# Kernel tuning notes

Measured on AMD Instinct MI355X. Metric: run time of the kernel, lower is better.

The kernel has to match this reference:

```python
import jax, jax.numpy as jnp
import numpy as np

N = 131072
DIMS_IN = 16
DIMS_C = 16
UNITS = 512
BINS = 10
MIN_W = 1e-3   # min_bin_width
MIN_H = 1e-3   # min_bin_height
MIN_D = 1e-3   # min_bin_derivative
N_PERMS = 4                 # ceil(log2(DIMS_IN))
BLOCKS = 2 * N_PERMS        # log permutation strategy doubles each bit-mask
DT = DIMS_IN // 2           # transformed dims per block (power-of-2 => exact half)
FEAT_IN = DT + DIMS_C       # subnet input features
FEAT_OUT = DT * (3 * BINS + 1)  # widths+heights+derivatives per transformed dim


def _masks():
    # Reproduces the 'log' permutation mask construction from Flow.__init__
    cm = np.array([[int(b) for b in np.binary_repr(j, N_PERMS)] for j in range(DIMS_IN)])
    cm = cm[:, ::-1].astype(bool).T           # (N_PERMS, DIMS_IN)
    m = np.repeat(cm, 2, axis=0)              # (BLOCKS, DIMS_IN)
    m[1::2] = ~m[1::2]
    return m  # True = condition dim, False = transformed dim


def _mlp(h, W0, b0, W1, b1, W2, b2):
    # layers=3 -> Linear/ReLU/Linear/ReLU/Linear
    h = jax.nn.relu(h @ W0 + b0)
    h = jax.nn.relu(h @ W1 + b1)
    return h @ W2 + b2


def _rqs_forward(x, uw, uh, ud):
    # x: (n, DT) in [0,1]; uw/uh: (n, DT, BINS); ud: (n, DT, BINS+1)
    w = MIN_W + (1.0 - MIN_W * BINS) * jax.nn.softmax(uw, axis=-1)
    h = MIN_H + (1.0 - MIN_H * BINS) * jax.nn.softmax(uh, axis=-1)
    d = MIN_D + jax.nn.softplus(ud)
    zero = jnp.zeros(w.shape[:-1] + (1,), w.dtype)
    cw = jnp.concatenate([zero, jnp.cumsum(w, axis=-1)], axis=-1)  # knot x-positions
    ch = jnp.concatenate([zero, jnp.cumsum(h, axis=-1)], axis=-1)  # knot y-positions
    # bin search: index of bin containing x
    idx = jnp.clip(jnp.sum(x[..., None] >= cw, axis=-1) - 1, 0, BINS - 1)
    take = lambda a, i: jnp.take_along_axis(a, i[..., None], axis=-1)[..., 0]
    xk, wk = take(cw, idx), take(w, idx)
    yk, hk = take(ch, idx), take(h, idx)
    dk, dk1 = take(d, idx), take(d, idx + 1)
    theta = jnp.clip((x - xk) / wk, 0.0, 1.0)
    s = hk / wk
    t1 = theta * (1.0 - theta)
    denom = s + (dk1 + dk - 2.0 * s) * t1
    y = yk + hk * (s * theta * theta + dk * t1) / denom
    logdet = (2.0 * jnp.log(s)
              + jnp.log(dk1 * theta * theta + 2.0 * s * t1 + dk * (1.0 - theta) ** 2)
              - 2.0 * jnp.log(denom))
    return y, logdet


def _log_prob(x, c, W0, b0, W1, b1, W2, b2):
    masks = _masks()
    z = x
    logdet = jnp.zeros(x.shape[0], x.dtype)
    for b in range(BLOCKS):
        m = masks[b]
        cond_idx = np.where(m)[0]
        trans_idx = np.where(~m)[0]
        subnet_in = jnp.concatenate([z[:, cond_idx], c], axis=-1)  # (n, FEAT_IN)
        params = _mlp(subnet_in, W0[b], b0[b], W1[b], b1[b], W2[b], b2[b])
        params = params.reshape(-1, DT, 3 * BINS + 1)
        uw, uh, ud = params[..., :BINS], params[..., BINS:2 * BINS], params[..., 2 * BINS:]
        y, lj = _rqs_forward(z[:, trans_idx], uw, uh, ud)
        logdet = logdet + jnp.sum(lj, axis=-1)
        z = z.at[:, trans_idx].set(y)
    # uniform latent on [0,1]^d => latent log-density is 0
    return logdet


def setup_inputs() -> dict:
    key = jax.random.key(0)
    ks = jax.random.split(key, 6)
    x = jax.random.uniform(ks[0], (N, DIMS_IN), jnp.float32)
    c = jax.random.normal(ks[1], (N, DIMS_C), jnp.float32)
    W0 = jax.random.normal(ks[2], (BLOCKS, FEAT_IN, UNITS), jnp.float32) / np.sqrt(FEAT_IN)
    W1 = jax.random.normal(ks[3], (BLOCKS, UNITS, UNITS), jnp.float32) / np.sqrt(UNITS)
    W2 = jax.random.normal(ks[4], (BLOCKS, UNITS, FEAT_OUT), jnp.float32) / np.sqrt(UNITS)
    b0 = jnp.zeros((BLOCKS, UNITS), jnp.float32)
    b1 = jnp.zeros((BLOCKS, UNITS), jnp.float32)
    b2 = jnp.zeros((BLOCKS, FEAT_OUT), jnp.float32)
    return {"x": x, "c": c, "W0": W0, "b0": b0, "W1": W1, "b1": b1, "W2": W2, "b2": b2}


def reference(x, c, W0, b0, W1, b1, W2, b2):
    return _log_prob(x, c, W0, b0, W1, b1, W2, b2)
```

## Files before the change

### kernel.cpp

```cpp
#include <hip/hip_runtime.h>
#include <math.h>

#define NROWS 131072
#define DIN   16
#define DC    16
#define UNITS 512
#define BINS  10
#define DT    8
#define FOUT  248
#define M_TILE 64
#define NWG   (NROWS / M_TILE)

#define Z_OFF    0u
#define W0F_OFF  8388608u
#define W1F_OFF  8650752u
#define W2F_OFF  12845056u

typedef _Float16 h16x8 __attribute__((ext_vector_type(8)));
typedef float    f32x4 __attribute__((ext_vector_type(4)));

union Frag { h16x8 v; uint4 q; unsigned int u32[4]; _Float16 h[8]; };

static __device__ inline unsigned int pack2h(float lo, float hi) {
    union { _Float16 h[2]; unsigned int u; } x;
    x.h[0] = (_Float16)lo; x.h[1] = (_Float16)hi;
    return x.u;
}

static __device__ inline float fast_rcp(float x) { return __builtin_amdgcn_rcpf(x); }

__global__ __launch_bounds__(256)
void prep_weights(const float* __restrict__ W0, const float* __restrict__ W1,
                  const float* __restrict__ W2, _Float16* __restrict__ W0F,
                  _Float16* __restrict__ W1F, _Float16* __restrict__ W2F)
{
    const int idx = blockIdx.x * 256 + threadIdx.x;
    const int SZ0 = 8 * 32 * 512;
    const int SZ1 = 8 * 32 * 16 * 512;
    const int SZ2 = 8 * 16 * 4 * 4 * 512;
    if (idx < SZ0) {
        int b = idx >> 14, r = idx & 16383;
        int ut = r >> 9, le = r & 511;
        int lane = le >> 3, j = le & 7;
        int quad = lane >> 4, l15 = lane & 15;
        int m = ut * 16 + l15, k = quad * 8 + j;
        W0F[idx] = (k < 24) ? (_Float16)W0[b * (24 * 512) + k * 512 + m] : (_Float16)0.f;
    } else if (idx < SZ0 + SZ1) {
        int i = idx - SZ0;
        int b = i >> 18, r = i & 262143;
        int ut = r >> 13, r2 = r & 8191;
        int ks = r2 >> 9, le = r2 & 511;
        int lane = le >> 3, j = le & 7;
        int quad = lane >> 4, l15 = lane & 15;
        int m = ut * 16 + l15, k = ks * 32 + quad * 8 + j;
        W1F[i] = (_Float16)W1[(b << 18) + k * 512 + m];
    } else if (idx < SZ0 + SZ1 + SZ2) {
        int i = idx - SZ0 - SZ1;
        int b = i >> 17, r = i & 131071;
        int ut2 = r >> 13, r2 = r & 8191;
        int c2 = r2 >> 11, r3 = r2 & 2047;
        int ks2 = r3 >> 9, le = r3 & 511;
        int lane = le >> 3, j = le & 7;
        int quad = lane >> 4, l15 = lane & 15;
        int m = ut2 * 16 + l15, k = c2 * 128 + ks2 * 32 + quad * 8 + j;
        W2F[i] = (m < FOUT) ? (_Float16)W2[b * (512 * FOUT) + k * FOUT + m] : (_Float16)0.f;
    }
}

__global__ __launch_bounds__(512, 4)
void flow_block_kernel(const float* __restrict__ z, const float* __restrict__ c,
                       const _Float16* __restrict__ W0F, const float* __restrict__ b0,
                       const _Float16* __restrict__ W1F, const float* __restrict__ b1,
                       const _Float16* __restrict__ W2F, const float* __restrict__ b2,
                       float* __restrict__ zout, float* __restrict__ logdet,
                       int p, int inv)
{
    __shared__ __align__(16) char smem[65536];

    const int t    = threadIdx.x;
    const int wave = t >> 6;
    const int lane = t & 63;
    const int quad = lane >> 4;
    const int l15  = lane & 15;
    const int row0 = blockIdx.x * M_TILE;
    const int lowmask = (1 << p) - 1;
    const int cv = 1 - inv, tv = inv;
    const int lofs = lane * 8;

    Frag bx[4];
    #pragma unroll
    for (int rt = 0; rt < 4; ++rt) {
        const int n = rt * 16 + l15;
        const float* zr = z + (size_t)(row0 + n) * DIN;
        const float* cr = c + (size_t)(row0 + n) * DC;
        float v[8];
        if (quad == 0) {
            #pragma unroll
            for (int j = 0; j < 8; ++j) {
                const int col = ((j >> p) << (p + 1)) | (cv << p) | (j & lowmask);
                v[j] = zr[col];
            }
        } else if (quad == 1) {
            #pragma unroll
            for (int j = 0; j < 8; ++j) v[j] = cr[j];
        } else if (quad == 2) {
            #pragma unroll
            for (int j = 0; j < 8; ++j) v[j] = cr[8 + j];
        } else {
            #pragma unroll
            for (int j = 0; j < 8; ++j) v[j] = 0.f;
        }
        #pragma unroll
        for (int j = 0; j < 4; ++j) bx[rt].u32[j] = pack2h(v[2 * j], v[2 * j + 1]);
    }

    #pragma unroll
    for (int j = 0; j < 4; ++j) {
        const int ut = wave * 4 + j;
        Frag a; a.q = *(const uint4*)(W0F + (ut << 9) + lofs);
        const f32x4 bias = *(const f32x4*)(b0 + ut * 16 + quad * 4);
        const int m0 = ut * 16 + quad * 4;
        #pragma unroll
        for (int rt = 0; rt < 4; ++rt) {
            f32x4 acc = __builtin_amdgcn_mfma_f32_16x16x32_f16(a.v, bx[rt].v, bias, 0, 0, 0);
            const int n = rt * 16 + l15;
            uint2 w2;
            w2.x = pack2h(fmaxf(acc.x, 0.f), fmaxf(acc.y, 0.f));
            w2.y = pack2h(fmaxf(acc.z, 0.f), fmaxf(acc.w, 0.f));
            const int addr = n * 1024 + (((m0 >> 3) ^ (n & 7)) * 16) + ((m0 & 4) * 2);
            *(uint2*)(smem + addr) = w2;
        }
    }
    __syncthreads();

    f32x4 h1[4][4];
    #pragma unroll
    for (int j = 0; j < 4; ++j) {
        const int ut = wave * 4 + j;
        const f32x4 bias = *(const f32x4*)(b1 + ut * 16 + quad * 4);
        #pragma unroll
        for (int rt = 0; rt < 4; ++rt) h1[j][rt] = bias;
    }
    #pragma unroll 2
    for (int ks = 0; ks < 16; ++ks) {
        Frag B[4];
        #pragma unroll
        for (int rt = 0; rt < 4; ++rt) {
            const int n = rt * 16 + l15;
            B[rt].v = *(const h16x8*)(smem + n * 1024 + (((ks * 4 + quad) ^ (n & 7)) * 16));
        }
        #pragma unroll
        for (int j = 0; j < 4; ++j) {
            const int ut = wave * 4 + j;
            Frag a; a.q = *(const uint4*)(W1F + (((ut << 4) + ks) << 9) + lofs);
            #pragma unroll
            for (int rt = 0; rt < 4; ++rt)
                h1[j][rt] = __builtin_amdgcn_mfma_f32_16x16x32_f16(a.v, B[rt].v, h1[j][rt], 0, 0, 0);
        }
    }
    __syncthreads();

    #pragma unroll
    for (int j = 0; j < 4; ++j) {
        const int ut = wave * 4 + j;
        const int m0 = ut * 16 + quad * 4;
        #pragma unroll
        for (int rt = 0; rt < 4; ++rt) {
            const int n = rt * 16 + l15;
            uint2 w2;
            w2.x = pack2h(fmaxf(h1[j][rt].x, 0.f), fmaxf(h1[j][rt].y, 0.f));
            w2.y = pack2h(fmaxf(h1[j][rt].z, 0.f), fmaxf(h1[j][rt].w, 0.f));
            const int addr = n * 1024 + (((m0 >> 3) ^ (n & 7)) * 16) + ((m0 & 4) * 2);
            *(uint2*)(smem + addr) = w2;
        }
    }
    __syncthreads();

    f32x4 pacc[2][4];
    #pragma unroll
    for (int i2 = 0; i2 < 2; ++i2) {
        const int m0 = (wave * 2 + i2) * 16 + quad * 4;
        f32x4 bias;
        if (m0 < FOUT) bias = *(const f32x4*)(b2 + m0);
        else { bias.x = 0.f; bias.y = 0.f; bias.z = 0.f; bias.w = 0.f; }
        #pragma unroll
        for (int rt = 0; rt < 4; ++rt) pacc[i2][rt] = bias;
    }
    #pragma unroll 2
    for (int kk = 0; kk < 16; ++kk) {
        const int kc = kk * 4 + quad;
        Frag B[4];
        #pragma unroll
        for (int rt = 0; rt < 4; ++rt) {
            const int n = rt * 16 + l15;
            B[rt].v = *(const h16x8*)(smem + n * 1024 + ((kc ^ (n & 7)) * 16));
        }
        #pragma unroll
        for (int i2 = 0; i2 < 2; ++i2) {
            const int ut2 = wave * 2 + i2;
            Frag a; a.q = *(const uint4*)(W2F + (((ut2 << 4) + kk) << 9) + lofs);
            #pragma unroll
            for (int rt = 0; rt < 4; ++rt)
                pacc[i2][rt] = __builtin_amdgcn_mfma_f32_16x16x32_f16(a.v, B[rt].v, pacc[i2][rt], 0, 0, 0);
        }
    }
    __syncthreads();

    #pragma unroll
    for (int i2 = 0; i2 < 2; ++i2) {
        const int m0 = (wave * 2 + i2) * 16 + quad * 4;
        if (m0 < FOUT) {
            #pragma unroll
            for (int rt = 0; rt < 4; ++rt) {
                const int n = rt * 16 + l15;
                *(f32x4*)(smem + n * 1008 + m0 * 4) = pacc[i2][rt];
            }
        }
    }
    __syncthreads();

    {
        const int r = t >> 3;
        const int d = t & 7;
        const int row = row0 + r;
        const int td = ((d >> p) << (p + 1)) | (tv << p) | (d & lowmask);

        const float x = z[(size_t)row * DIN + td];

        const float* pp = (const float*)(smem + r * 1008) + d * 31;
        float pv[31];
        #pragma unroll
        for (int i = 0; i < 31; ++i) pv[i] = pp[i];

        float mw = pv[0];
        #pragma unroll
        for (int i = 1; i < BINS; ++i) mw = fmaxf(mw, pv[i]);
        float w[BINS]; float sw = 0.f;
        #pragma unroll
        for (int i = 0; i < BINS; ++i) { w[i] = __expf(pv[i] - mw); sw += w[i]; }
        const float rw = (1.0f - 0.001f * BINS) * fast_rcp(sw);
        #pragma unroll
        for (int i = 0; i < BINS; ++i) w[i] = 0.001f + rw * w[i];

        float mh = pv[BINS];
        #pragma unroll
        for (int i = 1; i < BINS; ++i) mh = fmaxf(mh, pv[BINS + i]);
        float hh[BINS]; float sh = 0.f;
        #pragma unroll
        for (int i = 0; i < BINS; ++i) { hh[i] = __expf(pv[BINS + i] - mh); sh += hh[i]; }
        const float rh = (1.0f - 0.001f * BINS) * fast_rcp(sh);
        #pragma unroll
        for (int i = 0; i < BINS; ++i) hh[i] = 0.001f + rh * hh[i];

        float dd[BINS + 1];
        #pragma unroll
        for (int i = 0; i < BINS + 1; ++i) {
            const float u = pv[2 * BINS + i];
            dd[i] = 0.001f + fmaxf(u, 0.f) + __logf(1.f + __expf(-fabsf(u)));
        }

        float cw[BINS], ch[BINS];
        cw[0] = 0.f; ch[0] = 0.f;
        #pragma unroll
        for (int i = 0; i < BINS - 1; ++i) { cw[i + 1] = cw[i] + w[i]; ch[i + 1] = ch[i] + hh[i]; }

        float xk = cw[0], wk = w[0], yk = ch[0], hk = hh[0], dk = dd[0], dk1 = dd[1];
        #pragma unroll
        for (int i = 1; i < BINS; ++i) {
            const bool sel = (x >= cw[i]);
            xk  = sel ? cw[i]     : xk;
            wk  = sel ? w[i]      : wk;
            yk  = sel ? ch[i]     : yk;
            hk  = sel ? hh[i]     : hk;
            dk  = sel ? dd[i]     : dk;
            dk1 = sel ? dd[i + 1] : dk1;
        }

        const float inv_wk = fast_rcp(wk);
        float th = (x - xk) * inv_wk;
        th = fminf(fmaxf(th, 0.f), 1.f);
        const float s   = hk * inv_wk;
        const float t1  = th * (1.f - th);
        const float den = s + (dk1 + dk - 2.f * s) * t1;
        const float inv_den = fast_rcp(den);
        const float num = s * th * th + dk * t1;
        const float y   = yk + hk * num * inv_den;
        const float om  = 1.f - th;
        const float r1  = s * inv_den;
        const float q   = r1 * r1 * (dk1 * th * th + 2.f * s * t1 + dk * om * om);
        float ljv = __logf(q);

        zout[(size_t)row * DIN + td] = y;

        float v = ljv;
        v += __shfl_down(v, 4, 8);
        v += __shfl_down(v, 2, 8);
        v += __shfl_down(v, 1, 8);
        if ((t & 7) == 0) logdet[row0 + (t >> 3)] += v;
    }
}

extern "C" void kernel_launch(void* const* d_in, const int* in_sizes, int n_in,
                              void* d_out, int out_size, void* d_ws, size_t ws_size,
                              hipStream_t stream) {
    (void)in_sizes; (void)n_in; (void)out_size; (void)ws_size;
    const float* x  = (const float*)d_in[0];
    const float* c  = (const float*)d_in[1];
    const float* W0 = (const float*)d_in[2];
    const float* b0 = (const float*)d_in[3];
    const float* W1 = (const float*)d_in[4];
    const float* b1 = (const float*)d_in[5];
    const float* W2 = (const float*)d_in[6];
    const float* b2 = (const float*)d_in[7];
    float* out = (float*)d_out;

    char* ws = (char*)d_ws;
    float* z = (float*)(ws + Z_OFF);
    _Float16* W0F = (_Float16*)(ws + W0F_OFF);
    _Float16* W1F = (_Float16*)(ws + W1F_OFF);
    _Float16* W2F = (_Float16*)(ws + W2F_OFF);

    hipMemcpyAsync(z, x, (size_t)NROWS * DIN * sizeof(float),
                   hipMemcpyDeviceToDevice, stream);
    hipMemsetAsync(out, 0, (size_t)NROWS * sizeof(float), stream);

    prep_weights<<<12800, 256, 0, stream>>>(W0, W1, W2, W0F, W1F, W2F);

    dim3 grid(NWG), block(512);
    for (int b = 0; b < 8; ++b) {
        const int p = b >> 1, inv = b & 1;
        flow_block_kernel<<<grid, block, 0, stream>>>(
            z, c,
            W0F + (size_t)b * 32 * 512,          b0 + (size_t)b * UNITS,
            W1F + (size_t)b * 32 * 16 * 512,     b1 + (size_t)b * UNITS,
            W2F + (size_t)b * 16 * 4 * 4 * 512,  b2 + (size_t)b * FOUT,
            z, out, p, inv);
    }
}
```

Baseline: 1.087 ms.

## Fuse all eight flow blocks into one kernel with z held in LDS

Replaces the eight per-block kernel launches with a single kernel that loops over all coupling blocks. Each workgroup keeps its 64x16 z tile in shared memory, packs the conditioning inputs once, and accumulates logdet in registers, writing it once at the end. This removes the device-to-device copy, the memset, seven launches and the global z round trips between blocks. The cost is an extra LDS array on top of 64KB, which may reduce occupancy, plus a longer-running kernel per workgroup.

Result: slower. 1.208 ms (+11.1%).

```diff
diff --git a/kernel.cpp b/kernel.cpp
--- a/kernel.cpp
+++ b/kernel.cpp
@@ -11,10 +11,9 @@
 #define M_TILE 64
 #define NWG   (NROWS / M_TILE)
 
-#define Z_OFF    0u
-#define W0F_OFF  8388608u
-#define W1F_OFF  8650752u
-#define W2F_OFF  12845056u
+#define W0F_OFF  0u
+#define W1F_OFF  262144u
+#define W2F_OFF  4456448u
 
 typedef _Float16 h16x8 __attribute__((ext_vector_type(8)));
 typedef float    f32x4 __attribute__((ext_vector_type(4)));
@@ -68,14 +67,14 @@
 }
 
 __global__ __launch_bounds__(512, 4)
-void flow_block_kernel(const float* __restrict__ z, const float* __restrict__ c,
-                       const _Float16* __restrict__ W0F, const float* __restrict__ b0,
-                       const _Float16* __restrict__ W1F, const float* __restrict__ b1,
-                       const _Float16* __restrict__ W2F, const float* __restrict__ b2,
-                       float* __restrict__ zout, float* __restrict__ logdet,
-                       int p, int inv)
+void flow_fused(const float* __restrict__ x, const float* __restrict__ c,
+                const _Float16* __restrict__ W0F, const float* __restrict__ b0,
+                const _Float16* __restrict__ W1F, const float* __restrict__ b1,
+                const _Float16* __restrict__ W2F, const float* __restrict__ b2,
+                float* __restrict__ logdet)
 {
     __shared__ __align__(16) char smem[65536];
+    __shared__ float zt[64][17];
 
     const int t    = threadIdx.x;
     const int wave = t >> 6;
@@ -83,24 +82,22 @@
     const int quad = lane >> 4;
     const int l15  = lane & 15;
     const int row0 = blockIdx.x * M_TILE;
-    const int lowmask = (1 << p) - 1;
-    const int cv = 1 - inv, tv = inv;
     const int lofs = lane * 8;
 
-    Frag bx[4];
+    {
+        const float* xr = x + (size_t)row0 * DIN;
+        const int i0 = t, i1 = t + 512;
+        zt[i0 >> 4][i0 & 15] = xr[i0];
+        zt[i1 >> 4][i1 & 15] = xr[i1];
+    }
+
+    unsigned int cpk[4][4];
     #pragma unroll
     for (int rt = 0; rt < 4; ++rt) {
         const int n = rt * 16 + l15;
-        const float* zr = z + (size_t)(row0 + n) * DIN;
         const float* cr = c + (size_t)(row0 + n) * DC;
         float v[8];
-        if (quad == 0) {
-            #pragma unroll
-            for (int j = 0; j < 8; ++j) {
-                const int col = ((j >> p) << (p + 1)) | (cv << p) | (j & lowmask);
-                v[j] = zr[col];
-            }
-        } else if (quad == 1) {
+        if (quad == 1) {
             #pragma unroll
             for (int j = 0; j < 8; ++j) v[j] = cr[j];
         } else if (quad == 2) {
@@ -111,193 +108,229 @@
             for (int j = 0; j < 8; ++j) v[j] = 0.f;
         }
         #pragma unroll
-        for (int j = 0; j < 4; ++j) bx[rt].u32[j] = pack2h(v[2 * j], v[2 * j + 1]);
+        for (int j = 0; j < 4; ++j) cpk[rt][j] = pack2h(v[2 * j], v[2 * j + 1]);
     }
 
-    #pragma unroll
-    for (int j = 0; j < 4; ++j) {
-        const int ut = wave * 4 + j;
-        Frag a; a.q = *(const uint4*)(W0F + (ut << 9) + lofs);
-        const f32x4 bias = *(const f32x4*)(b0 + ut * 16 + quad * 4);
-        const int m0 = ut * 16 + quad * 4;
+    float ldacc = 0.f;
+    __syncthreads();
+
+    for (int b = 0; b < 8; ++b) {
+        const int p = b >> 1, inv = b & 1;
+        const int lowmask = (1 << p) - 1;
+        const int cv = 1 - inv, tv = inv;
+        const _Float16* W0Fb = W0F + (size_t)b * (32 * 512);
+        const _Float16* W1Fb = W1F + (size_t)b * (32 * 16 * 512);
+        const _Float16* W2Fb = W2F + (size_t)b * (16 * 4 * 4 * 512);
+        const float* b0b = b0 + b * UNITS;
+        const float* b1b = b1 + b * UNITS;
+        const float* b2b = b2 + b * FOUT;
+
+        Frag bx[4];
         #pragma unroll
         for (int rt = 0; rt < 4; ++rt) {
-            f32x4 acc = __builtin_amdgcn_mfma_f32_16x16x32_f16(a.v, bx[rt].v, bias, 0, 0, 0);
-            const int n = rt * 16 + l15;
-            uint2 w2;
-            w2.x = pack2h(fmaxf(acc.x, 0.f), fmaxf(acc.y, 0.f));
-            w2.y = pack2h(fmaxf(acc.z, 0.f), fmaxf(acc.w, 0.f));
-            const int addr = n * 1024 + (((m0 >> 3) ^ (n & 7)) * 16) + ((m0 & 4) * 2);
-            *(uint2*)(smem + addr) = w2;
-        }
-    }
-    __syncthreads();
-
-    f32x4 h1[4][4];
-    #pragma unroll
-    for (int j = 0; j < 4; ++j) {
-        const int ut = wave * 4 + j;
-        const f32x4 bias = *(const f32x4*)(b1 + ut * 16 + quad * 4);
-        #pragma unroll
-        for (int rt = 0; rt < 4; ++rt) h1[j][rt] = bias;
-    }
-    #pragma unroll 2
-    for (int ks = 0; ks < 16; ++ks) {
-        Frag B[4];
-        #pragma unroll
-        for (int rt = 0; rt < 4; ++rt) {
-            const int n = rt * 16 + l15;
-            B[rt].v = *(const h16x8*)(smem + n * 1024 + (((ks * 4 + quad) ^ (n & 7)) * 16));
-        }
+            if (quad == 0) {
+                const int n = rt * 16 + l15;
+                float v[8];
+                #pragma unroll
+                for (int j = 0; j < 8; ++j) {
+                    const int col = ((j >> p) << (p + 1)) | (cv << p) | (j & lowmask);
+                    v[j] = zt[n][col];
+                }
+                #pragma unroll
+                for (int j = 0; j < 4; ++j) bx[rt].u32[j] = pack2h(v[2 * j], v[2 * j + 1]);
+            } else {
+                #pragma unroll
+                for (int j = 0; j < 4; ++j) bx[rt].u32[j] = cpk[rt][j];
+            }
+        }
+
         #pragma unroll
         for (int j = 0; j < 4; ++j) {
             const int ut = wave * 4 + j;
-            Frag a; a.q = *(const uint4*)(W1F + (((ut << 4) + ks) << 9) + lofs);
-            #pragma unroll
-            for (int rt = 0; rt < 4; ++rt)
-                h1[j][rt] = __builtin_amdgcn_mfma_f32_16x16x32_f16(a.v, B[rt].v, h1[j][rt], 0, 0, 0);
-        }
+            Frag a; a.q = *(const uint4*)(W0Fb + (ut << 9) + lofs);
+            const f32x4 bias = *(const f32x4*)(b0b + ut * 16 + quad * 4);
+            const int m0 = ut * 16 + quad * 4;
+            #pragma unroll
+            for (int rt = 0; rt < 4; ++rt) {
+                f32x4 acc = __builtin_amdgcn_mfma_f32_16x16x32_f16(a.v, bx[rt].v, bias, 0, 0, 0);
+                const int n = rt * 16 + l15;
+                uint2 w2;
+                w2.x = pack2h(fmaxf(acc.x, 0.f), fmaxf(acc.y, 0.f));
+                w2.y = pack2h(fmaxf(acc.z, 0.f), fmaxf(acc.w, 0.f));
+                const int addr = n * 1024 + (((m0 >> 3) ^ (n & 7)) * 16) + ((m0 & 4) * 2);
+                *(uint2*)(smem + addr) = w2;
+            }
+        }
+        __syncthreads();
+
+        f32x4 h1[4][4];
+        #pragma unroll
+        for (int j = 0; j < 4; ++j) {
+            const int ut = wave * 4 + j;
+            const f32x4 bias = *(const f32x4*)(b1b + ut * 16 + quad * 4);
+            #pragma unroll
+            for (int rt = 0; rt < 4; ++rt) h1[j][rt] = bias;
+        }
+        #pragma unroll 2
+        for (int ks = 0; ks < 16; ++ks) {
+            Frag B[4];
+            #pragma unroll
+            for (int rt = 0; rt < 4; ++rt) {
+                const int n = rt * 16 + l15;
+                B[rt].v = *(const h16x8*)(smem + n * 1024 + (((ks * 4 + quad) ^ (n & 7)) * 16));
+            }
+            #pragma unroll
+            for (int j = 0; j < 4; ++j) {
+                const int ut = wave * 4 + j;
+                Frag a; a.q = *(const uint4*)(W1Fb + (((ut << 4) + ks) << 9) + lofs);
+                #pragma unroll
+                for (int rt = 0; rt < 4; ++rt)
+                    h1[j][rt] = __builtin_amdgcn_mfma_f32_16x16x32_f16(a.v, B[rt].v, h1[j][rt], 0, 0, 0);
+            }
+        }
+        __syncthreads();
+
+        #pragma unroll
+        for (int j = 0; j < 4; ++j) {
+            const int ut = wave * 4 + j;
+            const int m0 = ut * 16 + quad * 4;
+            #pragma unroll
+            for (int rt = 0; rt < 4; ++rt) {
+                const int n = rt * 16 + l15;
+                uint2 w2;
+                w2.x = pack2h(fmaxf(h1[j][rt].x, 0.f), fmaxf(h1[j][rt].y, 0.f));
+                w2.y = pack2h(fmaxf(h1[j][rt].z, 0.f), fmaxf(h1[j][rt].w, 0.f));
+                const int addr = n * 1024 + (((m0 >> 3) ^ (n & 7)) * 16) + ((m0 & 4) * 2);
+                *(uint2*)(smem + addr) = w2;
+            }
+        }
+        __syncthreads();
+
+        f32x4 pacc[2][4];
+        #pragma unroll
+        for (int i2 = 0; i2 < 2; ++i2) {
+            const int m0 = (wave * 2 + i2) * 16 + quad * 4;
+            f32x4 bias;
+            if (m0 < FOUT) bias = *(const f32x4*)(b2b + m0);
+            else { bias.x = 0.f; bias.y = 0.f; bias.z = 0.f; bias.w = 0.f; }
+            #pragma unroll
+            for (int rt = 0; rt < 4; ++rt) pacc[i2][rt] = bias;
+        }
+        #pragma unroll 2
+        for (int kk = 0; kk < 16; ++kk) {
+            const int kc = kk * 4 + quad;
+            Frag B[4];
+            #pragma unroll
+            for (int rt = 0; rt < 4; ++rt) {
+                const int n = rt * 16 + l15;
+                B[rt].v = *(const h16x8*)(smem + n * 1024 + ((kc ^ (n & 7)) * 16));
+            }
+            #pragma unroll
+            for (int i2 = 0; i2 < 2; ++i2) {
+                const int ut2 = wave * 2 + i2;
+                Frag a; a.q = *(const uint4*)(W2Fb + (((ut2 << 4) + kk) << 9) + lofs);
+                #pragma unroll
+                for (int rt = 0; rt < 4; ++rt)
+                    pacc[i2][rt] = __builtin_amdgcn_mfma_f32_16x16x32_f16(a.v, B[rt].v, pacc[i2][rt], 0, 0, 0);
+            }
+        }
+        __syncthreads();
+
+        #pragma unroll
+        for (int i2 = 0; i2 < 2; ++i2) {
+            const int m0 = (wave * 2 + i2) * 16 + quad * 4;
+            if (m0 < FOUT) {
+                #pragma unroll
+                for (int rt = 0; rt < 4; ++rt) {
+                    const int n = rt * 16 + l15;
+                    *(f32x4*)(smem + n * 1008 + m0 * 4) = pacc[i2][rt];
+                }
+            }
+        }
+        __syncthreads();
+
+        {
+            const int r = t >> 3;
+            const int d = t & 7;
+            const int td = ((d >> p) << (p + 1)) | (tv << p) | (d & lowmask);
+
+            const float xv = zt[r][td];
+
+            const float* pp = (const float*)(smem + r * 1008) + d * 31;
+            float pv[31];
+            #pragma unroll
+            for (int i = 0; i < 31; ++i) pv[i] = pp[i];
+
+            float mw = pv[0];
+            #pragma unroll
+            for (int i = 1; i < BINS; ++i) mw = fmaxf(mw, pv[i]);
+            float w[BINS]; float sw = 0.f;
+            #pragma unroll
+            for (int i = 0; i < BINS; ++i) { w[i] = __expf(pv[i] - mw); sw += w[i]; }
+            const float rw = (1.0f - 0.001f * BINS) * fast_rcp(sw);
+            #pragma unroll
+            for (int i = 0; i < BINS; ++i) w[i] = 0.001f + rw * w[i];
+
+            float mh = pv[BINS];
+            #pragma unroll
+            for (int i = 1; i < BINS; ++i) mh = fmaxf(mh, pv[BINS + i]);
+            float hh[BINS]; float sh = 0.f;
+            #pragma unroll
+            for (int i = 0; i < BINS; ++i) { hh[i] = __expf(pv[BINS + i] - mh); sh += hh[i]; }
+            const float rh = (1.0f - 0.001f * BINS) * fast_rcp(sh);
+            #pragma unroll
+            for (int i = 0; i < BINS; ++i) hh[i] = 0.001f + rh * hh[i];
+
+            float dd[BINS + 1];
+            #pragma unroll
+            for (int i = 0; i < BINS + 1; ++i) {
+                const float u = pv[2 * BINS + i];
+                dd[i] = 0.001f + fmaxf(u, 0.f) + __logf(1.f + __expf(-fabsf(u)));
+            }
+
+            float cw[BINS], ch[BINS];
+            cw[0] = 0.f; ch[0] = 0.f;
+            #pragma unroll
+            for (int i = 0; i < BINS - 1; ++i) { cw[i + 1] = cw[i] + w[i]; ch[i + 1] = ch[i] + hh[i]; }
+
+            float xk = cw[0], wk = w[0], yk = ch[0], hk = hh[0], dk = dd[0], dk1 = dd[1];
+            #pragma unroll
+            for (int i = 1; i < BINS; ++i) {
+                const bool sel = (xv >= cw[i]);
+                xk  = sel ? cw[i]     : xk;
+                wk  = sel ? w[i]      : wk;
+                yk  = sel ? ch[i]     : yk;
+                hk  = sel ? hh[i]     : hk;
+                dk  = sel ? dd[i]     : dk;
+                dk1 = sel ? dd[i + 1] : dk1;
+            }
+
+            const float inv_wk = fast_rcp(wk);
+            float th = (xv - xk) * inv_wk;
+            th = fminf(fmaxf(th, 0.f), 1.f);
+            const float s   = hk * inv_wk;
+            const float t1  = th * (1.f - th);
+            const float den = s + (dk1 + dk - 2.f * s) * t1;
+            const float inv_den = fast_rcp(den);
+            const float num = s * th * th + dk * t1;
+            const float y   = yk + hk * num * inv_den;
+            const float om  = 1.f - th;
+            const float r1  = s * inv_den;
+            const float q   = r1 * r1 * (dk1 * th * th + 2.f * s * t1 + dk * om * om);
+            float ljv = __logf(q);
+
+            zt[r][td] = y;
+
+            float v = ljv;
+            v += __shfl_down(v, 4, 8);
+            v += __shfl_down(v, 2, 8);
+            v += __shfl_down(v, 1, 8);
+            if ((t & 7) == 0) ldacc += v;
+        }
+        __syncthreads();
     }
-    __syncthreads();
-
-    #pragma unroll
-    for (int j = 0; j < 4; ++j) {
-        const int ut = wave * 4 + j;
-        const int m0 = ut * 16 + quad * 4;
-        #pragma unroll
-        for (int rt = 0; rt < 4; ++rt) {
-            const int n = rt * 16 + l15;
-            uint2 w2;
-            w2.x = pack2h(fmaxf(h1[j][rt].x, 0.f), fmaxf(h1[j][rt].y, 0.f));
-            w2.y = pack2h(fmaxf(h1[j][rt].z, 0.f), fmaxf(h1[j][rt].w, 0.f));
-            const int addr = n * 1024 + (((m0 >> 3) ^ (n & 7)) * 16) + ((m0 & 4) * 2);
-            *(uint2*)(smem + addr) = w2;
-        }
-    }
-    __syncthreads();
-
-    f32x4 pacc[2][4];
-    #pragma unroll
-    for (int i2 = 0; i2 < 2; ++i2) {
-        const int m0 = (wave * 2 + i2) * 16 + quad * 4;
-        f32x4 bias;
-        if (m0 < FOUT) bias = *(const f32x4*)(b2 + m0);
-        else { bias.x = 0.f; bias.y = 0.f; bias.z = 0.f; bias.w = 0.f; }
-        #pragma unroll
-        for (int rt = 0; rt < 4; ++rt) pacc[i2][rt] = bias;
-    }
-    #pragma unroll 2
-    for (int kk = 0; kk < 16; ++kk) {
-        const int kc = kk * 4 + quad;
-        Frag B[4];
-        #pragma unroll
-        for (int rt = 0; rt < 4; ++rt) {
-            const int n = rt * 16 + l15;
-            B[rt].v = *(const h16x8*)(smem + n * 1024 + ((kc ^ (n & 7)) * 16));
-        }
-        #pragma unroll
-        for (int i2 = 0; i2 < 2; ++i2) {
-            const int ut2 = wave * 2 + i2;
-            Frag a; a.q = *(const uint4*)(W2F + (((ut2 << 4) + kk) << 9) + lofs);
-            #pragma unroll
-            for (int rt = 0; rt < 4; ++rt)
-                pacc[i2][rt] = __builtin_amdgcn_mfma_f32_16x16x32_f16(a.v, B[rt].v, pacc[i2][rt], 0, 0, 0);
-        }
-    }
-    __syncthreads();
-
-    #pragma unroll
-    for (int i2 = 0; i2 < 2; ++i2) {
-        const int m0 = (wave * 2 + i2) * 16 + quad * 4;
-        if (m0 < FOUT) {
-            #pragma unroll
-            for (int rt = 0; rt < 4; ++rt) {
-                const int n = rt * 16 + l15;
-                *(f32x4*)(smem + n * 1008 + m0 * 4) = pacc[i2][rt];
-            }
-        }
-    }
-    __syncthreads();
-
-    {
-        const int r = t >> 3;
-        const int d = t & 7;
-        const int row = row0 + r;
-        const int td = ((d >> p) << (p + 1)) | (tv << p) | (d & lowmask);
-
-        const float x = z[(size_t)row * DIN + td];
-
-        const float* pp = (const float*)(smem + r * 1008) + d * 31;
-        float pv[31];
-        #pragma unroll
-        for (int i = 0; i < 31; ++i) pv[i] = pp[i];
-
-        float mw = pv[0];
-        #pragma unroll
-        for (int i = 1; i < BINS; ++i) mw = fmaxf(mw, pv[i]);
-        float w[BINS]; float sw = 0.f;
-        #pragma unroll
-        for (int i = 0; i < BINS; ++i) { w[i] = __expf(pv[i] - mw); sw += w[i]; }
-        const float rw = (1.0f - 0.001f * BINS) * fast_rcp(sw);
-        #pragma unroll
-        for (int i = 0; i < BINS; ++i) w[i] = 0.001f + rw * w[i];
-
-        float mh = pv[BINS];
-        #pragma unroll
-        for (int i = 1; i < BINS; ++i) mh = fmaxf(mh, pv[BINS + i]);
-        float hh[BINS]; float sh = 0.f;
-        #pragma unroll
-        for (int i = 0; i < BINS; ++i) { hh[i] = __expf(pv[BINS + i] - mh); sh += hh[i]; }
-        const float rh = (1.0f - 0.001f * BINS) * fast_rcp(sh);
-        #pragma unroll
-        for (int i = 0; i < BINS; ++i) hh[i] = 0.001f + rh * hh[i];
-
-        float dd[BINS + 1];
-        #pragma unroll
-        for (int i = 0; i < BINS + 1; ++i) {
-            const float u = pv[2 * BINS + i];
-            dd[i] = 0.001f + fmaxf(u, 0.f) + __logf(1.f + __expf(-fabsf(u)));
-        }
-
-        float cw[BINS], ch[BINS];
-        cw[0] = 0.f; ch[0] = 0.f;
-        #pragma unroll
-        for (int i = 0; i < BINS - 1; ++i) { cw[i + 1] = cw[i] + w[i]; ch[i + 1] = ch[i] + hh[i]; }
-
-        float xk = cw[0], wk = w[0], yk = ch[0], hk = hh[0], dk = dd[0], dk1 = dd[1];
-        #pragma unroll
-        for (int i = 1; i < BINS; ++i) {
-            const bool sel = (x >= cw[i]);
-            xk  = sel ? cw[i]     : xk;
-            wk  = sel ? w[i]      : wk;
-            yk  = sel ? ch[i]     : yk;
-            hk  = sel ? hh[i]     : hk;
-            dk  = sel ? dd[i]     : dk;
-            dk1 = sel ? dd[i + 1] : dk1;
-        }
-
-        const float inv_wk = fast_rcp(wk);
-        float th = (x - xk) * inv_wk;
-        th = fminf(fmaxf(th, 0.f), 1.f);
-        const float s   = hk * inv_wk;
-        const float t1  = th * (1.f - th);
-        const float den = s + (dk1 + dk - 2.f * s) * t1;
-        const float inv_den = fast_rcp(den);
-        const float num = s * th * th + dk * t1;
-        const float y   = yk + hk * num * inv_den;
-        const float om  = 1.f - th;
-        const float r1  = s * inv_den;
-        const float q   = r1 * r1 * (dk1 * th * th + 2.f * s * t1 + dk * om * om);
-        float ljv = __logf(q);
-
-        zout[(size_t)row * DIN + td] = y;
-
-        float v = ljv;
-        v += __shfl_down(v, 4, 8);
-        v += __shfl_down(v, 2, 8);
-        v += __shfl_down(v, 1, 8);
-        if ((t & 7) == 0) logdet[row0 + (t >> 3)] += v;
-    }
+
+    if ((t & 7) == 0) logdet[row0 + (t >> 3)] = ldacc;
 }
 
 extern "C" void kernel_launch(void* const* d_in, const int* in_sizes, int n_in,
@@ -315,25 +348,12 @@
     float* out = (float*)d_out;
 
     char* ws = (char*)d_ws;
-    float* z = (float*)(ws + Z_OFF);
     _Float16* W0F = (_Float16*)(ws + W0F_OFF);
     _Float16* W1F = (_Float16*)(ws + W1F_OFF);
     _Float16* W2F = (_Float16*)(ws + W2F_OFF);
 
-    hipMemcpyAsync(z, x, (size_t)NROWS * DIN * sizeof(float),
-                   hipMemcpyDeviceToDevice, stream);
-    hipMemsetAsync(out, 0, (size_t)NROWS * sizeof(float), stream);
-
     prep_weights<<<12800, 256, 0, stream>>>(W0, W1, W2, W0F, W1F, W2F);
 
-    dim3 grid(NWG), block(512);
-    for (int b = 0; b < 8; ++b) {
-        const int p = b >> 1, inv = b & 1;
-        flow_block_kernel<<<grid, block, 0, stream>>>(
-            z, c,
-            W0F + (size_t)b * 32 * 512,          b0 + (size_t)b * UNITS,
-            W1F + (size_t)b * 32 * 16 * 512,     b1 + (size_t)b * UNITS,
-            W2F + (size_t)b * 16 * 4 * 4 * 512,  b2 + (size_t)b * FOUT,
-            z, out, p, inv);
-    }
+    flow_fused<<<dim3(NWG), dim3(512), 0, stream>>>(
+        x, c, W0F, b0, W1F, b1, W2F, b2, out);
 }
```

## Fuse all eight flow blocks into one persistent kernel with MFMA priority hints

Applied to the files above, without the earlier changes.

Replaces the eight per-block kernel launches with a single persistent kernel of 512 workgroups. Each workgroup owns a fixed set of row tiles and loops over all eight coupling blocks. Because each row's data dependency stays inside one workgroup, no grid-wide sync is needed, and launch gaps and tail effects between blocks go away. It also wraps the MFMA inner loops in s_setprio. The trade-off is less parallelism: 512 workgroups of 512 threads, each processing four tiles serially per block, may underfill the GPU compared with 2048 workgroups per launch.

Measured after the change: 1.469 ms. 1.35x slower.

```diff
diff --git a/kernel.cpp b/kernel.cpp
--- a/kernel.cpp
+++ b/kernel.cpp
@@ -9,7 +9,9 @@
 #define DT    8
 #define FOUT  248
 #define M_TILE 64
-#define NWG   (NROWS / M_TILE)
+#define NTILES (NROWS / M_TILE)
+#define PWG   512
+#define TPW   (NTILES / PWG)
 
 #define Z_OFF    0u
 #define W0F_OFF  8388608u
@@ -68,12 +70,11 @@
 }
 
 __global__ __launch_bounds__(512, 4)
-void flow_block_kernel(const float* __restrict__ z, const float* __restrict__ c,
-                       const _Float16* __restrict__ W0F, const float* __restrict__ b0,
-                       const _Float16* __restrict__ W1F, const float* __restrict__ b1,
-                       const _Float16* __restrict__ W2F, const float* __restrict__ b2,
-                       float* __restrict__ zout, float* __restrict__ logdet,
-                       int p, int inv)
+void flow_persist(const float* __restrict__ zin, const float* __restrict__ c,
+                  const _Float16* __restrict__ W0F, const float* __restrict__ b0,
+                  const _Float16* __restrict__ W1F, const float* __restrict__ b1,
+                  const _Float16* __restrict__ W2F, const float* __restrict__ b2,
+                  float* __restrict__ zout, float* __restrict__ logdet)
 {
     __shared__ __align__(16) char smem[65536];
 
@@ -82,221 +83,239 @@
     const int lane = t & 63;
     const int quad = lane >> 4;
     const int l15  = lane & 15;
-    const int row0 = blockIdx.x * M_TILE;
-    const int lowmask = (1 << p) - 1;
-    const int cv = 1 - inv, tv = inv;
     const int lofs = lane * 8;
 
-    Frag bx[4];
-    #pragma unroll
-    for (int rt = 0; rt < 4; ++rt) {
-        const int n = rt * 16 + l15;
-        const float* zr = z + (size_t)(row0 + n) * DIN;
-        const float* cr = c + (size_t)(row0 + n) * DC;
-        float v[8];
-        if (quad == 0) {
-            #pragma unroll
-            for (int j = 0; j < 8; ++j) {
-                const int col = ((j >> p) << (p + 1)) | (cv << p) | (j & lowmask);
-                v[j] = zr[col];
-            }
-        } else if (quad == 1) {
-            #pragma unroll
-            for (int j = 0; j < 8; ++j) v[j] = cr[j];
-        } else if (quad == 2) {
-            #pragma unroll
-            for (int j = 0; j < 8; ++j) v[j] = cr[8 + j];
-        } else {
-            #pragma unroll
-            for (int j = 0; j < 8; ++j) v[j] = 0.f;
-        }
-        #pragma unroll
-        for (int j = 0; j < 4; ++j) bx[rt].u32[j] = pack2h(v[2 * j], v[2 * j + 1]);
-    }
-
-    #pragma unroll
-    for (int j = 0; j < 4; ++j) {
-        const int ut = wave * 4 + j;
-        Frag a; a.q = *(const uint4*)(W0F + (ut << 9) + lofs);
-        const f32x4 bias = *(const f32x4*)(b0 + ut * 16 + quad * 4);
-        const int m0 = ut * 16 + quad * 4;
-        #pragma unroll
-        for (int rt = 0; rt < 4; ++rt) {
-            f32x4 acc = __builtin_amdgcn_mfma_f32_16x16x32_f16(a.v, bx[rt].v, bias, 0, 0, 0);
-            const int n = rt * 16 + l15;
-            uint2 w2;
-            w2.x = pack2h(fmaxf(acc.x, 0.f), fmaxf(acc.y, 0.f));
-            w2.y = pack2h(fmaxf(acc.z, 0.f), fmaxf(acc.w, 0.f));
-            const int addr = n * 1024 + (((m0 >> 3) ^ (n & 7)) * 16) + ((m0 & 4) * 2);
-            *(uint2*)(smem + addr) = w2;
-        }
-    }
-    __syncthreads();
-
-    f32x4 h1[4][4];
-    #pragma unroll
-    for (int j = 0; j < 4; ++j) {
-        const int ut = wave * 4 + j;
-        const f32x4 bias = *(const f32x4*)(b1 + ut * 16 + quad * 4);
-        #pragma unroll
-        for (int rt = 0; rt < 4; ++rt) h1[j][rt] = bias;
-    }
-    #pragma unroll 2
-    for (int ks = 0; ks < 16; ++ks) {
-        Frag B[4];
-        #pragma unroll
-        for (int rt = 0; rt < 4; ++rt) {
-            const int n = rt * 16 + l15;
-            B[rt].v = *(const h16x8*)(smem + n * 1024 + (((ks * 4 + quad) ^ (n & 7)) * 16));
-        }
-        #pragma unroll
-        for (int j = 0; j < 4; ++j) {
-            const int ut = wave * 4 + j;
-            Frag a; a.q = *(const uint4*)(W1F + (((ut << 4) + ks) << 9) + lofs);
-            #pragma unroll
-            for (int rt = 0; rt < 4; ++rt)
-                h1[j][rt] = __builtin_amdgcn_mfma_f32_16x16x32_f16(a.v, B[rt].v, h1[j][rt], 0, 0, 0);
-        }
-    }
-    __syncthreads();
-
-    #pragma unroll
-    for (int j = 0; j < 4; ++j) {
-        const int ut = wave * 4 + j;
-        const int m0 = ut * 16 + quad * 4;
-        #pragma unroll
-        for (int rt = 0; rt < 4; ++rt) {
-            const int n = rt * 16 + l15;
-            uint2 w2;
-            w2.x = pack2h(fmaxf(h1[j][rt].x, 0.f), fmaxf(h1[j][rt].y, 0.f));
-            w2.y = pack2h(fmaxf(h1[j][rt].z, 0.f), fmaxf(h1[j][rt].w, 0.f));
-            const int addr = n * 1024 + (((m0 >> 3) ^ (n & 7)) * 16) + ((m0 & 4) * 2);
-            *(uint2*)(smem + addr) = w2;
-        }
-    }
-    __syncthreads();
-
-    f32x4 pacc[2][4];
-    #pragma unroll
-    for (int i2 = 0; i2 < 2; ++i2) {
-        const int m0 = (wave * 2 + i2) * 16 + quad * 4;
-        f32x4 bias;
-        if (m0 < FOUT) bias = *(const f32x4*)(b2 + m0);
-        else { bias.x = 0.f; bias.y = 0.f; bias.z = 0.f; bias.w = 0.f; }
-        #pragma unroll
-        for (int rt = 0; rt < 4; ++rt) pacc[i2][rt] = bias;
-    }
-    #pragma unroll 2
-    for (int kk = 0; kk < 16; ++kk) {
-        const int kc = kk * 4 + quad;
-        Frag B[4];
-        #pragma unroll
-        for (int rt = 0; rt < 4; ++rt) {
-            const int n = rt * 16 + l15;
-            B[rt].v = *(const h16x8*)(smem + n * 1024 + ((kc ^ (n & 7)) * 16));
-        }
-        #pragma unroll
-        for (int i2 = 0; i2 < 2; ++i2) {
-            const int ut2 = wave * 2 + i2;
-            Frag a; a.q = *(const uint4*)(W2F + (((ut2 << 4) + kk) << 9) + lofs);
-            #pragma unroll
-            for (int rt = 0; rt < 4; ++rt)
-                pacc[i2][rt] = __builtin_amdgcn_mfma_f32_16x16x32_f16(a.v, B[rt].v, pacc[i2][rt], 0, 0, 0);
-        }
-    }
-    __syncthreads();
-
-    #pragma unroll
-    for (int i2 = 0; i2 < 2; ++i2) {
-        const int m0 = (wave * 2 + i2) * 16 + quad * 4;
-        if (m0 < FOUT) {
+    for (int b = 0; b < 8; ++b) {
+        const int p = b >> 1, inv = b & 1;
+        const int lowmask = (1 << p) - 1;
+        const int cv = 1 - inv, tv = inv;
+        const _Float16* W0Fb = W0F + (size_t)b * (32 * 512);
+        const _Float16* W1Fb = W1F + (size_t)b * (32 * 16 * 512);
+        const _Float16* W2Fb = W2F + (size_t)b * (16 * 4 * 4 * 512);
+        const float* b0b = b0 + b * UNITS;
+        const float* b1b = b1 + b * UNITS;
+        const float* b2b = b2 + b * FOUT;
+
+        for (int tt = 0; tt < TPW; ++tt) {
+            const int row0 = (blockIdx.x + tt * PWG) * M_TILE;
+
+            Frag bx[4];
             #pragma unroll
             for (int rt = 0; rt < 4; ++rt) {
                 const int n = rt * 16 + l15;
-                *(f32x4*)(smem + n * 1008 + m0 * 4) = pacc[i2][rt];
-            }
+                const float* zr = zin + (size_t)(row0 + n) * DIN;
+                const float* cr = c + (size_t)(row0 + n) * DC;
+                float v[8];
+                if (quad == 0) {
+                    #pragma unroll
+                    for (int j = 0; j < 8; ++j) {
+                        const int col = ((j >> p) << (p + 1)) | (cv << p) | (j & lowmask);
+                        v[j] = zr[col];
+                    }
+                } else if (quad == 1) {
+                    #pragma unroll
+                    for (int j = 0; j < 8; ++j) v[j] = cr[j];
+                } else if (quad == 2) {
+                    #pragma unroll
+                    for (int j = 0; j < 8; ++j) v[j] = cr[8 + j];
+                } else {
+                    #pragma unroll
+                    for (int j = 0; j < 8; ++j) v[j] = 0.f;
+                }
+                #pragma unroll
+                for (int j = 0; j < 4; ++j) bx[rt].u32[j] = pack2h(v[2 * j], v[2 * j + 1]);
+            }
+
+            #pragma unroll
+            for (int j = 0; j < 4; ++j) {
+                const int ut = wave * 4 + j;
+                Frag a; a.q = *(const uint4*)(W0Fb + (ut << 9) + lofs);
+                const f32x4 bias = *(const f32x4*)(b0b + ut * 16 + quad * 4);
+                const int m0 = ut * 16 + quad * 4;
+                #pragma unroll
+                for (int rt = 0; rt < 4; ++rt) {
+                    f32x4 acc = __builtin_amdgcn_mfma_f32_16x16x32_f16(a.v, bx[rt].v, bias, 0, 0, 0);
+                    const int n = rt * 16 + l15;
+                    uint2 w2;
+                    w2.x = pack2h(fmaxf(acc.x, 0.f), fmaxf(acc.y, 0.f));
+                    w2.y = pack2h(fmaxf(acc.z, 0.f), fmaxf(acc.w, 0.f));
+                    const int addr = n * 1024 + (((m0 >> 3) ^ (n & 7)) * 16) + ((m0 & 4) * 2);
+                    *(uint2*)(smem + addr) = w2;
+                }
+            }
+            __syncthreads();
+
+            f32x4 h1[4][4];
+            #pragma unroll
+            for (int j = 0; j < 4; ++j) {
+                const int ut = wave * 4 + j;
+                const f32x4 bias = *(const f32x4*)(b1b + ut * 16 + quad * 4);
+                #pragma unroll
+                for (int rt = 0; rt < 4; ++rt) h1[j][rt] = bias;
+            }
+            #pragma unroll 2
+            for (int ks = 0; ks < 16; ++ks) {
+                Frag B[4];
+                #pragma unroll
+                for (int rt = 0; rt < 4; ++rt) {
+                    const int n = rt * 16 + l15;
+                    B[rt].v = *(const h16x8*)(smem + n * 1024 + (((ks * 4 + quad) ^ (n & 7)) * 16));
+                }
+                __builtin_amdgcn_s_setprio(1);
+                #pragma unroll
+                for (int j = 0; j < 4; ++j) {
+                    const int ut = wave * 4 + j;
+                    Frag a; a.q = *(const uint4*)(W1Fb + (((ut << 4) + ks) << 9) + lofs);
+                    #pragma unroll
+                    for (int rt = 0; rt < 4; ++rt)
+                        h1[j][rt] = __builtin_amdgcn_mfma_f32_16x16x32_f16(a.v, B[rt].v, h1[j][rt], 0, 0, 0);
+                }
+                __builtin_amdgcn_s_setprio(0);
+            }
+            __syncthreads();
+
+            #pragma unroll
+            for (int j = 0; j < 4; ++j) {
+                const int ut = wave * 4 + j;
+                const int m0 = ut * 16 + quad * 4;
+                #pragma unroll
+                for (int rt = 0; rt < 4; ++rt) {
+                    const int n = rt * 16 + l15;
+                    uint2 w2;
+                    w2.x = pack2h(fmaxf(h1[j][rt].x, 0.f), fmaxf(h1[j][rt].y, 0.f));
+                    w2.y = pack2h(fmaxf(h1[j][rt].z, 0.f), fmaxf(h1[j][rt].w, 0.f));
+                    const int addr = n * 1024 + (((m0 >> 3) ^ (n & 7)) * 16) + ((m0 & 4) * 2);
+                    *(uint2*)(smem + addr) = w2;
+                }
+            }
+            __syncthreads();
+
+            f32x4 pacc[2][4];
+            #pragma unroll
+            for (int i2 = 0; i2 < 2; ++i2) {
+                const int m0 = (wave * 2 + i2) * 16 + quad * 4;
+                f32x4 bias;
+                if (m0 < FOUT) bias = *(const f32x4*)(b2b + m0);
+                else { bias.x = 0.f; bias.y = 0.f; bias.z = 0.f; bias.w = 0.f; }
+                #pragma unroll
+                for (int rt = 0; rt < 4; ++rt) pacc[i2][rt] = bias;
+            }
+            #pragma unroll 2
+            for (int kk = 0; kk < 16; ++kk) {
+                const int kc = kk * 4 + quad;
+                Frag B[4];
+                #pragma unroll
+                for (int rt = 0; rt < 4; ++rt) {
+                    const int n = rt * 16 + l15;
+                    B[rt].v = *(const h16x8*)(smem + n * 1024 + ((kc ^ (n & 7)) * 16));
+                }
+                __builtin_amdgcn_s_setprio(1);
+                #pragma unroll
+                for (int i2 = 0; i2 < 2; ++i2) {
+                    const int ut2 = wave * 2 + i2;
+                    Frag a; a.q = *(const uint4*)(W2Fb + (((ut2 << 4) + kk) << 9) + lofs);
+                    #pragma unroll
+                    for (int rt = 0; rt < 4; ++rt)
+                        pacc[i2][rt] = __builtin_amdgcn_mfma_f32_16x16x32_f16(a.v, B[rt].v, pacc[i2][rt], 0, 0, 0);
+                }
+                __builtin_amdgcn_s_setprio(0);
+            }
+            __syncthreads();
+
+            #pragma unroll
+            for (int i2 = 0; i2 < 2; ++i2) {
+                const int m0 = (wave * 2 + i2) * 16 + quad * 4;
+                if (m0 < FOUT) {
+                    #pragma unroll
+                    for (int rt = 0; rt < 4; ++rt) {
+                        const int n = rt * 16 + l15;
+                        *(f32x4*)(smem + n * 1008 + m0 * 4) = pacc[i2][rt];
+                    }
+                }
+            }
+            __syncthreads();
+
+            {
+                const int r = t >> 3;
+                const int d = t & 7;
+                const int row = row0 + r;
+                const int td = ((d >> p) << (p + 1)) | (tv << p) | (d & lowmask);
+
+                const float x = zin[(size_t)row * DIN + td];
+
+                const float* pp = (const float*)(smem + r * 1008) + d * 31;
+                float pv[31];
+                #pragma unroll
+                for (int i = 0; i < 31; ++i) pv[i] = pp[i];
+
+                float mw = pv[0];
+                #pragma unroll
+                for (int i = 1; i < BINS; ++i) mw = fmaxf(mw, pv[i]);
+                float w[BINS]; float sw = 0.f;
+                #pragma unroll
+                for (int i = 0; i < BINS; ++i) { w[i] = __expf(pv[i] - mw); sw += w[i]; }
+                const float rw = (1.0f - 0.001f * BINS) * fast_rcp(sw);
+                #pragma unroll
+                for (int i = 0; i < BINS; ++i) w[i] = 0.001f + rw * w[i];
+
+                float mh = pv[BINS];
+                #pragma unroll
+                for (int i = 1; i < BINS; ++i) mh = fmaxf(mh, pv[BINS + i]);
+                float hh[BINS]; float sh = 0.f;
+                #pragma unroll
+                for (int i = 0; i < BINS; ++i) { hh[i] = __expf(pv[BINS + i] - mh); sh += hh[i]; }
+                const float rh = (1.0f - 0.001f * BINS) * fast_rcp(sh);
+                #pragma unroll
+                for (int i = 0; i < BINS; ++i) hh[i] = 0.001f + rh * hh[i];
+
+                float dd[BINS + 1];
+                #pragma unroll
+                for (int i = 0; i < BINS + 1; ++i) {
+                    const float u = pv[2 * BINS + i];
+                    dd[i] = 0.001f + fmaxf(u, 0.f) + __logf(1.f + __expf(-fabsf(u)));
+                }
+
+                float cw[BINS], ch[BINS];
+                cw[0] = 0.f; ch[0] = 0.f;
+                #pragma unroll
+                for (int i = 0; i < BINS - 1; ++i) { cw[i + 1] = cw[i] + w[i]; ch[i + 1] = ch[i] + hh[i]; }
+
+                float xk = cw[0], wk = w[0], yk = ch[0], hk = hh[0], dk = dd[0], dk1 = dd[1];
+                #pragma unroll
+                for (int i = 1; i < BINS; ++i) {
+                    const bool sel = (x >= cw[i]);
+                    xk  = sel ? cw[i]     : xk;
+                    wk  = sel ? w[i]      : wk;
+                    yk  = sel ? ch[i]     : yk;
+                    hk  = sel ? hh[i]     : hk;
+                    dk  = sel ? dd[i]     : dk;
+                    dk1 = sel ? dd[i + 1] : dk1;
+                }
+
+                const float inv_wk = fast_rcp(wk);
+                float th = (x - xk) * inv_wk;
+                th = fminf(fmaxf(th, 0.f), 1.f);
+                const float s   = hk * inv_wk;
+                const float t1  = th * (1.f - th);
+                const float den = s + (dk1 + dk - 2.f * s) * t1;
+                const float inv_den = fast_rcp(den);
+                const float num = s * th * th + dk * t1;
+                const float y   = yk + hk * num * inv_den;
+                const float om  = 1.f - th;
+                const float r1  = s * inv_den;
+                const float q   = r1 * r1 * (dk1 * th * th + 2.f * s * t1 + dk * om * om);
+                float ljv = __logf(q);
+
+                zout[(size_t)row * DIN + td] = y;
+
+                float v = ljv;
+                v += __shfl_down(v, 4, 8);
+                v += __shfl_down(v, 2, 8);
+                v += __shfl_down(v, 1, 8);
+                if ((t & 7) == 0) logdet[row] += v;
+            }
+            __syncthreads();
         }
-    }
-    __syncthreads();
-
-    {
-        const int r = t >> 3;
-        const int d = t & 7;
-        const int row = row0 + r;
-        const int td = ((d >> p) << (p + 1)) | (tv << p) | (d & lowmask);
-
-        const float x = z[(size_t)row * DIN + td];
-
-        const float* pp = (const float*)(smem + r * 1008) + d * 31;
-        float pv[31];
-        #pragma unroll
-        for (int i = 0; i < 31; ++i) pv[i] = pp[i];
-
-        float mw = pv[0];
-        #pragma unroll
-        for (int i = 1; i < BINS; ++i) mw = fmaxf(mw, pv[i]);
-        float w[BINS]; float sw = 0.f;
-        #pragma unroll
-        for (int i = 0; i < BINS; ++i) { w[i] = __expf(pv[i] - mw); sw += w[i]; }
-        const float rw = (1.0f - 0.001f * BINS) * fast_rcp(sw);
-        #pragma unroll
-        for (int i = 0; i < BINS; ++i) w[i] = 0.001f + rw * w[i];
-
-        float mh = pv[BINS];
-        #pragma unroll
-        for (int i = 1; i < BINS; ++i) mh = fmaxf(mh, pv[BINS + i]);
-        float hh[BINS]; float sh = 0.f;
-        #pragma unroll
-        for (int i = 0; i < BINS; ++i) { hh[i] = __expf(pv[BINS + i] - mh); sh += hh[i]; }
-        const float rh = (1.0f - 0.001f * BINS) * fast_rcp(sh);
-        #pragma unroll
-        for (int i = 0; i < BINS; ++i) hh[i] = 0.001f + rh * hh[i];
-
-        float dd[BINS + 1];
-        #pragma unroll
-        for (int i = 0; i < BINS + 1; ++i) {
-            const float u = pv[2 * BINS + i];
-            dd[i] = 0.001f + fmaxf(u, 0.f) + __logf(1.f + __expf(-fabsf(u)));
-        }
-
-        float cw[BINS], ch[BINS];
-        cw[0] = 0.f; ch[0] = 0.f;
-        #pragma unroll
-        for (int i = 0; i < BINS - 1; ++i) { cw[i + 1] = cw[i] + w[i]; ch[i + 1] = ch[i] + hh[i]; }
-
-        float xk = cw[0], wk = w[0], yk = ch[0], hk = hh[0], dk = dd[0], dk1 = dd[1];
-        #pragma unroll
-        for (int i = 1; i < BINS; ++i) {
-            const bool sel = (x >= cw[i]);
-            xk  = sel ? cw[i]     : xk;
-            wk  = sel ? w[i]      : wk;
-            yk  = sel ? ch[i]     : yk;
-            hk  = sel ? hh[i]     : hk;
-            dk  = sel ? dd[i]     : dk;
-            dk1 = sel ? dd[i + 1] : dk1;
-        }
-
-        const float inv_wk = fast_rcp(wk);
-        float th = (x - xk) * inv_wk;
-        th = fminf(fmaxf(th, 0.f), 1.f);
-        const float s   = hk * inv_wk;
-        const float t1  = th * (1.f - th);
-        const float den = s + (dk1 + dk - 2.f * s) * t1;
-        const float inv_den = fast_rcp(den);
-        const float num = s * th * th + dk * t1;
-        const float y   = yk + hk * num * inv_den;
-        const float om  = 1.f - th;
-        const float r1  = s * inv_den;
-        const float q   = r1 * r1 * (dk1 * th * th + 2.f * s * t1 + dk * om * om);
-        float ljv = __logf(q);
-
-        zout[(size_t)row * DIN + td] = y;
-
-        float v = ljv;
-        v += __shfl_down(v, 4, 8);
-        v += __shfl_down(v, 2, 8);
-        v += __shfl_down(v, 1, 8);
-        if ((t & 7) == 0) logdet[row0 + (t >> 3)] += v;
     }
 }
 
@@ -326,14 +345,6 @@
 
     prep_weights<<<12800, 256, 0, stream>>>(W0, W1, W2, W0F, W1F, W2F);
 
-    dim3 grid(NWG), block(512);
-    for (int b = 0; b < 8; ++b) {
-        const int p = b >> 1, inv = b & 1;
-        flow_block_kernel<<<grid, block, 0, stream>>>(
-            z, c,
-            W0F + (size_t)b * 32 * 512,          b0 + (size_t)b * UNITS,
-            W1F + (size_t)b * 32 * 16 * 512,     b1 + (size_t)b * UNITS,
-            W2F + (size_t)b * 16 * 4 * 4 * 512,  b2 + (size_t)b * FOUT,
-            z, out, p, inv);
-    }
+    flow_persist<<<dim3(PWG), dim3(512), 0, stream>>>(
+        z, c, W0F, b0, W1F, b1, W2F, b2, z, out);
 }
```
